# Kernel tuning notes

Hardware: AMD Instinct MI355X
Metric: run time of the kernel (lower is better)

The kernel has to match this reference:

```python
import jax, jax.numpy as jnp
from jax import lax
import numpy as np

NOTES = 78
IN_DIM = 80
T_HID = 64
N_HID = 2
B = 64
T = 128


def lstm_seq(x, w_ih, w_hh, b_ih, b_hh):
    """Batch-first single-layer LSTM from zero state.
    x: (N, S, D); w_ih: (4H, D); w_hh: (4H, H). Gate order i,f,g,o (PyTorch).
    Returns hidden outputs (N, S, H)."""
    H = w_hh.shape[1]
    N = x.shape[0]
    # precompute input contribution for all steps: (N, S, 4H)
    gx = jnp.einsum('nsd,gd->nsg', x, w_ih) + b_ih + b_hh

    def step(carry, g_t):
        h, c = carry
        g = g_t + h @ w_hh.T
        i, f, gg, o = jnp.split(g, 4, axis=-1)
        c = jax.nn.sigmoid(f) * c + jax.nn.sigmoid(i) * jnp.tanh(gg)
        h = jax.nn.sigmoid(o) * jnp.tanh(c)
        return (h, c), h

    h0 = jnp.zeros((N, H), x.dtype)
    (_, _), hs = lax.scan(step, (h0, h0), jnp.swapaxes(gx, 0, 1))
    return jnp.swapaxes(hs, 0, 1)  # (N, S, H)


def setup_inputs() -> dict:
    key = jax.random.key(0)
    ks = jax.random.split(key, 9)
    s = 1.0 / np.sqrt(T_HID)
    sn = 1.0 / np.sqrt(N_HID)
    u = lambda k, shp, sc: jax.random.uniform(k, shp, jnp.float32, -sc, sc)
    return {
        'x': jax.random.normal(ks[0], (B, NOTES, T, IN_DIM), jnp.float32),
        'w_ih_t': u(ks[1], (4 * T_HID, IN_DIM), s),
        'w_hh_t': u(ks[2], (4 * T_HID, T_HID), s),
        'b_ih_t': u(ks[3], (4 * T_HID,), s),
        'b_hh_t': u(ks[4], (4 * T_HID,), s),
        'w_ih_n': u(ks[5], (4 * N_HID, T_HID), sn),
        'w_hh_n': u(ks[6], (4 * N_HID, N_HID), sn),
        'b_ih_n': u(ks[7], (4 * N_HID,), sn),
        'b_hh_n': u(ks[8], (4 * N_HID,), sn),
    }


def reference(x, w_ih_t, w_hh_t, b_ih_t, b_hh_t, w_ih_n, w_hh_n, b_ih_n, b_hh_n):
    b, n_notes, t_len, _ = x.shape
    # Time LSTM: independent over (batch, note); sequence axis = time.
    xt = x.reshape(b * n_notes, t_len, IN_DIM)
    time_out = lstm_seq(xt, w_ih_t, w_hh_t, b_ih_t, b_hh_t)  # (B*78, T, H)
    time_out = time_out.reshape(b, n_notes, t_len, T_HID)
    # Note LSTM: run over the 78-note axis, fresh zero state at EVERY time step
    # (faithful to the original, which reuses self.hidden_note0 each iteration).
    xn = jnp.transpose(time_out, (0, 2, 1, 3)).reshape(b * t_len, n_notes, T_HID)
    note_out = lstm_seq(xn, w_ih_n, w_hh_n, b_ih_n, b_hh_n)  # (B*T, 78, 2)
    note_out = note_out.reshape(b, t_len, n_notes * N_HID)  # (B, T, 156)
    # Hard threshold, exactly as torch.where(x > 0.5, ones, zeros)
    return jnp.where(note_out > 0.5, jnp.ones_like(note_out), jnp.zeros_like(note_out))
```

## Files before the change

### kernel.cpp

```cpp
#include <hip/hip_runtime.h>
#include <math.h>

#define NOTES 78
#define IN_DIM 80
#define T_HID 64
#define N_HID 2
#define BATCH 64
#define TLEN 128
#define NSEQ (BATCH * NOTES)
#define NBT  (BATCH * TLEN)
#define SB   8

__device__ __forceinline__ float sigf(float x) {
    return 1.0f / (1.0f + expf(-x));
}

__global__ __launch_bounds__(512, 1)
void time_lstm_fused(const float* __restrict__ x,
                     const float* __restrict__ w_ih,
                     const float* __restrict__ w_hh,
                     const float* __restrict__ b_ih,
                     const float* __restrict__ b_hh,
                     const float* __restrict__ w_ih_n,
                     const float* __restrict__ b_ih_n,
                     const float* __restrict__ b_hh_n,
                     float* __restrict__ gxn) {
    __shared__ __align__(16) float xbuf[SB][IN_DIM];
    __shared__ __align__(16) float hbuf[SB][T_HID];
    __shared__ float G0[SB][256];
    __shared__ float G1[SB][256];

    const int tid  = threadIdx.x;
    const int s0   = blockIdx.x * SB;
    const int g    = tid & 255;
    const int half = tid >> 8;

    float4 w[20];
    if (half == 0) {
        const float4* p = (const float4*)(w_ih + (size_t)g * IN_DIM);
#pragma unroll
        for (int j = 0; j < 20; j++) w[j] = p[j];
    } else {
        const float4* p = (const float4*)(w_hh + (size_t)g * T_HID);
#pragma unroll
        for (int j = 0; j < 16; j++) w[j] = p[j];
    }
    const float bias = (half == 0) ? (b_ih[g] + b_hh[g]) : 0.0f;

    const int su = tid >> 6;
    const int uu = tid & 63;
    float cst = 0.0f;

    const int nj = (tid >> 3) & 7;
    const int nk = tid & 7;
    float wn[8];
#pragma unroll
    for (int i = 0; i < 8; i++) wn[i] = w_ih_n[nj * 64 + nk * 8 + i];
    const float nbias = b_ih_n[nj] + b_hh_n[nj];
    const int sglb = s0 + su;
    const int nb = sglb / NOTES, nn = sglb % NOTES;
    float* gout = gxn + ((size_t)nn * NBT + (size_t)nb * TLEN) * 8 + nj;

    const int pls = tid / 20;
    const int pj  = tid % 20;

    hbuf[su][uu] = 0.0f;
    if (tid < SB * 20) {
        ((float4*)xbuf[pls])[pj] =
            *(const float4*)(x + ((size_t)(s0 + pls) * TLEN) * IN_DIM + 4 * pj);
    }
    __syncthreads();

    for (int t = 0; t < TLEN; t++) {
        float4 xp;
        const bool pf = (t + 1 < TLEN) && (tid < SB * 20);
        if (pf) {
            xp = *(const float4*)(x + ((size_t)(s0 + pls) * TLEN + (t + 1)) * IN_DIM + 4 * pj);
        }

        if (t > 0) {
            float p = 0.0f;
#pragma unroll
            for (int i = 0; i < 8; i++) p = fmaf(wn[i], hbuf[su][nk * 8 + i], p);
            p += __shfl_xor(p, 1);
            p += __shfl_xor(p, 2);
            p += __shfl_xor(p, 4);
            if (nk == 0) gout[(size_t)(t - 1) * 8] = p + nbias;
        }

        float acc[SB];
#pragma unroll
        for (int s = 0; s < SB; s++) acc[s] = bias;
        if (half == 0) {
#pragma unroll
            for (int j = 0; j < 20; j++) {
                const float4 wv = w[j];
#pragma unroll
                for (int s = 0; s < SB; s++) {
                    const float4 v = ((const float4*)xbuf[s])[j];
                    acc[s] = fmaf(wv.w, v.w, fmaf(wv.z, v.z,
                             fmaf(wv.y, v.y, fmaf(wv.x, v.x, acc[s]))));
                }
            }
            float* Gp = &G0[0][0];
#pragma unroll
            for (int s = 0; s < SB; s++) Gp[s * 256 + g] = acc[s];
        } else {
#pragma unroll
            for (int j = 0; j < 16; j++) {
                const float4 wv = w[j];
#pragma unroll
                for (int s = 0; s < SB; s++) {
                    const float4 v = ((const float4*)hbuf[s])[j];
                    acc[s] = fmaf(wv.w, v.w, fmaf(wv.z, v.z,
                             fmaf(wv.y, v.y, fmaf(wv.x, v.x, acc[s]))));
                }
            }
            float* Gp = &G1[0][0];
#pragma unroll
            for (int s = 0; s < SB; s++) Gp[s * 256 + g] = acc[s];
        }
        __syncthreads();

        {
            const float i_p = G0[su][uu]        + G1[su][uu];
            const float f_p = G0[su][64 + uu]   + G1[su][64 + uu];
            const float g_p = G0[su][128 + uu]  + G1[su][128 + uu];
            const float o_p = G0[su][192 + uu]  + G1[su][192 + uu];
            const float iv = sigf(i_p);
            const float fv = sigf(f_p);
            const float gv = tanhf(g_p);
            const float ov = sigf(o_p);
            cst = fv * cst + iv * gv;
            const float h = ov * tanhf(cst);
            hbuf[su][uu] = h;
        }
        if (pf) ((float4*)xbuf[pls])[pj] = xp;
        __syncthreads();
    }

    {
        float p = 0.0f;
#pragma unroll
        for (int i = 0; i < 8; i++) p = fmaf(wn[i], hbuf[su][nk * 8 + i], p);
        p += __shfl_xor(p, 1);
        p += __shfl_xor(p, 2);
        p += __shfl_xor(p, 4);
        if (nk == 0) gout[(size_t)(TLEN - 1) * 8] = p + nbias;
    }
}

__global__ __launch_bounds__(64)
void note_scan_kernel(const float* __restrict__ gxn,
                      const float* __restrict__ w_hh_n,
                      float* __restrict__ out) {
    const int bt = blockIdx.x * 64 + threadIdx.x;
    float wh[16];
#pragma unroll
    for (int i = 0; i < 16; i++) wh[i] = w_hh_n[i];
    float h0 = 0.f, h1 = 0.f, c0 = 0.f, c1 = 0.f;

    const float4* gp = (const float4*)gxn;
    float* op = out + (size_t)bt * (NOTES * N_HID);

    size_t idx = (size_t)bt * 2;
    float4 ga = gp[idx], gb = gp[idx + 1];
    for (int n = 0; n < NOTES; n++) {
        float4 na, nb2;
        if (n + 1 < NOTES) {
            const size_t nidx = ((size_t)(n + 1) * NBT + bt) * 2;
            na  = gp[nidx];
            nb2 = gp[nidx + 1];
        }
        const float i0 = ga.x + wh[0]  * h0 + wh[1]  * h1;
        const float i1 = ga.y + wh[2]  * h0 + wh[3]  * h1;
        const float f0 = ga.z + wh[4]  * h0 + wh[5]  * h1;
        const float f1 = ga.w + wh[6]  * h0 + wh[7]  * h1;
        const float g0 = gb.x + wh[8]  * h0 + wh[9]  * h1;
        const float g1 = gb.y + wh[10] * h0 + wh[11] * h1;
        const float o0 = gb.z + wh[12] * h0 + wh[13] * h1;
        const float o1 = gb.w + wh[14] * h0 + wh[15] * h1;
        c0 = sigf(f0) * c0 + sigf(i0) * tanhf(g0);
        c1 = sigf(f1) * c1 + sigf(i1) * tanhf(g1);
        h0 = sigf(o0) * tanhf(c0);
        h1 = sigf(o1) * tanhf(c1);
        op[n * 2 + 0] = (h0 > 0.5f) ? 1.0f : 0.0f;
        op[n * 2 + 1] = (h1 > 0.5f) ? 1.0f : 0.0f;
        ga = na; gb = nb2;
    }
}

extern "C" void kernel_launch(void* const* d_in, const int* in_sizes, int n_in,
                              void* d_out, int out_size, void* d_ws, size_t ws_size,
                              hipStream_t stream) {
    const float* x      = (const float*)d_in[0];
    const float* w_ih_t = (const float*)d_in[1];
    const float* w_hh_t = (const float*)d_in[2];
    const float* b_ih_t = (const float*)d_in[3];
    const float* b_hh_t = (const float*)d_in[4];
    const float* w_ih_n = (const float*)d_in[5];
    const float* w_hh_n = (const float*)d_in[6];
    const float* b_ih_n = (const float*)d_in[7];
    const float* b_hh_n = (const float*)d_in[8];
    float* out = (float*)d_out;

    float* gxn = (float*)d_ws;

    time_lstm_fused<<<NSEQ / SB, 512, 0, stream>>>(
        x, w_ih_t, w_hh_t, b_ih_t, b_hh_t, w_ih_n, b_ih_n, b_hh_n, gxn);
    note_scan_kernel<<<NBT / 64, 64, 0, stream>>>(gxn, w_hh_n, out);
}
```

Baseline: 1.433 ms.

## Read x directly from global, broadcast h via readlane, batch note-scan stores

The time LSTM kernel drops the shared-memory x staging buffer and its prefetch, and instead reads x straight from global memory inside the input projection loop. The recurrent half now loads one h value per lane and broadcasts it across the wavefront with readlane instead of issuing float4 LDS reads. The launch bound is raised so up to four blocks can share a CU. The note scan keeps its 156 thresholded outputs in a register array and writes them at the end as float4 stores. The aims are less LDS traffic and fewer scattered global stores, at the cost of many redundant global x loads per thread, a large number of readlane instructions, and higher register pressure that the wider launch bound may turn into spills.

```diff
diff --git a/kernel.cpp b/kernel.cpp
--- a/kernel.cpp
+++ b/kernel.cpp
@@ -14,8 +14,11 @@
 __device__ __forceinline__ float sigf(float x) {
     return 1.0f / (1.0f + expf(-x));
 }
-
-__global__ __launch_bounds__(512, 1)
+__device__ __forceinline__ float rdlane(float v, int k) {
+    return __int_as_float(__builtin_amdgcn_readlane(__float_as_int(v), k));
+}
+
+__global__ __launch_bounds__(512, 4)
 void time_lstm_fused(const float* __restrict__ x,
                      const float* __restrict__ w_ih,
                      const float* __restrict__ w_hh,
@@ -25,7 +28,6 @@
                      const float* __restrict__ b_ih_n,
                      const float* __restrict__ b_hh_n,
                      float* __restrict__ gxn) {
-    __shared__ __align__(16) float xbuf[SB][IN_DIM];
     __shared__ __align__(16) float hbuf[SB][T_HID];
     __shared__ float G0[SB][256];
     __shared__ float G1[SB][256];
@@ -34,6 +36,7 @@
     const int s0   = blockIdx.x * SB;
     const int g    = tid & 255;
     const int half = tid >> 8;
+    const int lane = tid & 63;
 
     float4 w[20];
     if (half == 0) {
@@ -46,6 +49,11 @@
         for (int j = 0; j < 16; j++) w[j] = p[j];
     }
     const float bias = (half == 0) ? (b_ih[g] + b_hh[g]) : 0.0f;
+
+    const float* xs[SB];
+#pragma unroll
+    for (int s = 0; s < SB; s++)
+        xs[s] = x + ((size_t)(s0 + s) * TLEN) * IN_DIM;
 
     const int su = tid >> 6;
     const int uu = tid & 63;
@@ -61,23 +69,10 @@
     const int nb = sglb / NOTES, nn = sglb % NOTES;
     float* gout = gxn + ((size_t)nn * NBT + (size_t)nb * TLEN) * 8 + nj;
 
-    const int pls = tid / 20;
-    const int pj  = tid % 20;
-
     hbuf[su][uu] = 0.0f;
-    if (tid < SB * 20) {
-        ((float4*)xbuf[pls])[pj] =
-            *(const float4*)(x + ((size_t)(s0 + pls) * TLEN) * IN_DIM + 4 * pj);
-    }
     __syncthreads();
 
     for (int t = 0; t < TLEN; t++) {
-        float4 xp;
-        const bool pf = (t + 1 < TLEN) && (tid < SB * 20);
-        if (pf) {
-            xp = *(const float4*)(x + ((size_t)(s0 + pls) * TLEN + (t + 1)) * IN_DIM + 4 * pj);
-        }
-
         if (t > 0) {
             float p = 0.0f;
 #pragma unroll
@@ -89,31 +84,39 @@
         }
 
         float acc[SB];
-#pragma unroll
-        for (int s = 0; s < SB; s++) acc[s] = bias;
         if (half == 0) {
+#pragma unroll
+            for (int s = 0; s < SB; s++) acc[s] = bias;
 #pragma unroll
             for (int j = 0; j < 20; j++) {
                 const float4 wv = w[j];
 #pragma unroll
                 for (int s = 0; s < SB; s++) {
-                    const float4 v = ((const float4*)xbuf[s])[j];
-                    acc[s] = fmaf(wv.w, v.w, fmaf(wv.z, v.z,
-                             fmaf(wv.y, v.y, fmaf(wv.x, v.x, acc[s]))));
+                    const float4 xv = *(const float4*)(xs[s] + (size_t)t * IN_DIM + 4 * j);
+                    acc[s] = fmaf(wv.w, xv.w, fmaf(wv.z, xv.z,
+                             fmaf(wv.y, xv.y, fmaf(wv.x, xv.x, acc[s]))));
                 }
             }
             float* Gp = &G0[0][0];
 #pragma unroll
             for (int s = 0; s < SB; s++) Gp[s * 256 + g] = acc[s];
         } else {
-#pragma unroll
-            for (int j = 0; j < 16; j++) {
-                const float4 wv = w[j];
+            float hv[SB];
+#pragma unroll
+            for (int s = 0; s < SB; s++) hv[s] = hbuf[s][lane];
+#pragma unroll
+            for (int s = 0; s < SB; s++) acc[s] = 0.0f;
+#pragma unroll
+            for (int k4 = 0; k4 < 16; k4++) {
+                const float4 wv = w[k4];
 #pragma unroll
                 for (int s = 0; s < SB; s++) {
-                    const float4 v = ((const float4*)hbuf[s])[j];
-                    acc[s] = fmaf(wv.w, v.w, fmaf(wv.z, v.z,
-                             fmaf(wv.y, v.y, fmaf(wv.x, v.x, acc[s]))));
+                    const float h0 = rdlane(hv[s], 4 * k4 + 0);
+                    const float h1 = rdlane(hv[s], 4 * k4 + 1);
+                    const float h2 = rdlane(hv[s], 4 * k4 + 2);
+                    const float h3 = rdlane(hv[s], 4 * k4 + 3);
+                    acc[s] = fmaf(wv.w, h3, fmaf(wv.z, h2,
+                             fmaf(wv.y, h1, fmaf(wv.x, h0, acc[s]))));
                 }
             }
             float* Gp = &G1[0][0];
@@ -135,7 +138,6 @@
             const float h = ov * tanhf(cst);
             hbuf[su][uu] = h;
         }
-        if (pf) ((float4*)xbuf[pls])[pj] = xp;
         __syncthreads();
     }
 
@@ -161,7 +163,7 @@
     float h0 = 0.f, h1 = 0.f, c0 = 0.f, c1 = 0.f;
 
     const float4* gp = (const float4*)gxn;
-    float* op = out + (size_t)bt * (NOTES * N_HID);
+    float res[2 * NOTES];
 
     size_t idx = (size_t)bt * 2;
     float4 ga = gp[idx], gb = gp[idx + 1];
@@ -184,9 +186,14 @@
         c1 = sigf(f1) * c1 + sigf(i1) * tanhf(g1);
         h0 = sigf(o0) * tanhf(c0);
         h1 = sigf(o1) * tanhf(c1);
-        op[n * 2 + 0] = (h0 > 0.5f) ? 1.0f : 0.0f;
-        op[n * 2 + 1] = (h1 > 0.5f) ? 1.0f : 0.0f;
+        res[n * 2 + 0] = (h0 > 0.5f) ? 1.0f : 0.0f;
+        res[n * 2 + 1] = (h1 > 0.5f) ? 1.0f : 0.0f;
         ga = na; gb = nb2;
+    }
+    float4* op = (float4*)(out + (size_t)bt * (NOTES * N_HID));
+#pragma unroll
+    for (int j = 0; j < (2 * NOTES) / 4; j++) {
+        op[j] = make_float4(res[4 * j], res[4 * j + 1], res[4 * j + 2], res[4 * j + 3]);
     }
 }
 
```

Measured after the change: 2.576 ms. 79.8% more time.
